# Optimization experiments

Hardware: AMD Instinct MI355X
Metric: run time of the kernel (lower is better)

The kernel has to match this reference:

```python
import jax, jax.numpy as jnp
import numpy as np

N_NODES = 100000
N_EDGES = 1600000
F_IN = 32
HID = 64


def _gcn_conv(x, edge_index, edge_weight, W, b):
    """PyG GCNConv with edge_weight: add self-loops, symmetric degree norm, scatter-add."""
    N = x.shape[0]
    xw = x @ W  # [N, out]
    row, col = edge_index[0], edge_index[1]
    loop = jnp.arange(N)
    row = jnp.concatenate([row, loop])
    col = jnp.concatenate([col, loop])
    ew = jnp.concatenate([edge_weight, jnp.ones((N,), dtype=x.dtype)])
    # degree on target nodes
    deg = jax.ops.segment_sum(ew, col, num_segments=N)
    dinv = jnp.where(deg > 0, jax.lax.rsqrt(deg), 0.0)
    norm = dinv[row] * ew * dinv[col]  # [E+N]
    msg = norm[:, None] * xw[row]      # gather + scale over edges
    out = jax.ops.segment_sum(msg, col, num_segments=N)  # scatter-add
    return out + b


def setup_inputs() -> dict:
    key = jax.random.key(0)
    k = jax.random.split(key, 8)
    x = jax.random.normal(k[0], (N_NODES, F_IN), dtype=jnp.float32)
    edge_index = jax.random.randint(k[1], (2, N_EDGES), 0, N_NODES, dtype=jnp.int64)
    edge_attr = jax.random.uniform(k[2], (N_EDGES, 1), dtype=jnp.float32)
    s1 = 1.0 / np.sqrt(F_IN)
    s2 = 1.0 / np.sqrt(HID)
    W1 = jax.random.normal(k[3], (F_IN, HID), dtype=jnp.float32) * s1
    b1 = jnp.zeros((HID,), dtype=jnp.float32)
    W2 = jax.random.normal(k[4], (HID, F_IN), dtype=jnp.float32) * s2
    b2 = jnp.zeros((F_IN,), dtype=jnp.float32)
    return {"x": x, "edge_index": edge_index, "edge_attr": edge_attr,
            "W1": W1, "b1": b1, "W2": W2, "b2": b2}


def reference(x, edge_index, edge_attr, W1, b1, W2, b2):
    ew = edge_attr.squeeze(-1)
    h = jax.nn.relu(_gcn_conv(x, edge_index, ew, W1, b1))
    out = jax.nn.relu(_gcn_conv(h, edge_index, ew, W2, b2))
    return (out, edge_attr)
```

## Files before the change

kernel.cpp:

```cpp
#include <hip/hip_runtime.h>

#define NN 100000
#define NE 1600000
#define FIN 32
#define FHID 64

#define CLB 7
#define BN (1 << CLB)
#define NB ((NN + BN - 1) / BN)
#define NDB 256
#define CHUNK ((NE + NDB - 1) / NDB)
#define NSC (NB * NDB)
#define SCAN_B 1024
#define SCAN_NB ((NSC + SCAN_B - 1) / SCAN_B)

#define LGKM0 asm volatile("s_waitcnt lgkmcnt(0)" ::: "memory")

__device__ __forceinline__ float lo16(unsigned g) {
    return __uint_as_float(g << 16);
}
__device__ __forceinline__ float hi16(unsigned g) {
    return __uint_as_float(g & 0xFFFF0000u);
}
__device__ __forceinline__ unsigned pack_bf16(float a, float b) {
    unsigned ua = __float_as_uint(a);
    unsigned ub = __float_as_uint(b);
    ua += 0x7FFFu + ((ua >> 16) & 1u);
    ub += 0x7FFFu + ((ub >> 16) & 1u);
    return (ua >> 16) | (ub & 0xFFFF0000u);
}

__global__ void k_dcount(const int* __restrict__ col, int* __restrict__ hist_g) {
    __shared__ int hc[NB];
    for (int i = threadIdx.x; i < NB; i += blockDim.x) hc[i] = 0;
    __syncthreads();
    int beg = blockIdx.x * CHUNK, end = min(beg + CHUNK, NE);
    for (int e = beg + threadIdx.x; e < end; e += blockDim.x)
        atomicAdd(&hc[col[e] >> CLB], 1);
    __syncthreads();
    for (int i = threadIdx.x; i < NB; i += blockDim.x)
        hist_g[i * NDB + blockIdx.x] = hc[i];
}

__global__ void k_scan1(const int* __restrict__ in, int* __restrict__ out,
                        int* __restrict__ bsum) {
    __shared__ int s[SCAN_B];
    int i = blockIdx.x * SCAN_B + threadIdx.x;
    int v = (i < NSC) ? in[i] : 0;
    s[threadIdx.x] = v;
    __syncthreads();
    for (int o = 1; o < SCAN_B; o <<= 1) {
        int t = (threadIdx.x >= o) ? s[threadIdx.x - o] : 0;
        __syncthreads();
        s[threadIdx.x] += t;
        __syncthreads();
    }
    if (i < NSC) out[i] = s[threadIdx.x] - v;
    if (threadIdx.x == SCAN_B - 1) bsum[blockIdx.x] = s[SCAN_B - 1];
}

__global__ void k_scan2(int* __restrict__ bsum) {
    __shared__ int s[256];
    int v = (threadIdx.x < SCAN_NB) ? bsum[threadIdx.x] : 0;
    s[threadIdx.x] = v;
    __syncthreads();
    for (int o = 1; o < 256; o <<= 1) {
        int t = (threadIdx.x >= o) ? s[threadIdx.x - o] : 0;
        __syncthreads();
        s[threadIdx.x] += t;
        __syncthreads();
    }
    if (threadIdx.x < SCAN_NB) bsum[threadIdx.x] = s[threadIdx.x] - v;
}

__global__ void k_scan3(int* __restrict__ out, const int* __restrict__ bsum) {
    int i = blockIdx.x * blockDim.x + threadIdx.x;
    if (i < NSC) out[i] += bsum[i >> 10];
}

__global__ void k_dwrite(const int* __restrict__ row, const int* __restrict__ col,
                         const float* __restrict__ ew, const int* __restrict__ base_g,
                         uint2* __restrict__ rec0) {
    __shared__ int rk[NB];
    __shared__ int bl[NB];
    for (int i = threadIdx.x; i < NB; i += blockDim.x) {
        rk[i] = 0;
        bl[i] = base_g[i * NDB + blockIdx.x];
    }
    __syncthreads();
    int beg = blockIdx.x * CHUNK, end = min(beg + CHUNK, NE);
    for (int e = beg + threadIdx.x; e < end; e += blockDim.x) {
        int c = col[e];
        int bk = c >> CLB;
        int r = atomicAdd(&rk[bk], 1);
        unsigned pack = ((unsigned)(c & (BN - 1)) << 17) | (unsigned)row[e];
        rec0[bl[bk] + r] = make_uint2(pack, __float_as_uint(ew[e]));
    }
}

__global__ void k_bsort(const int* __restrict__ base_g, const uint2* __restrict__ rec0,
                        uint2* __restrict__ csr, int* __restrict__ rowptr,
                        float* __restrict__ dinv) {
    __shared__ int cnt[BN];
    __shared__ int bas[BN];
    __shared__ int cur[BN];
    __shared__ float dg[BN];
    int tid = threadIdx.x;
    int b = blockIdx.x;
    int beg = base_g[b * NDB];
    int end = (b == NB - 1) ? NE : base_g[(b + 1) * NDB];
    if (tid < BN) { cnt[tid] = 0; dg[tid] = 0.0f; }
    __syncthreads();
    for (int j = beg + tid; j < end; j += blockDim.x) {
        uint2 p = rec0[j];
        int cl = p.x >> 17;
        atomicAdd(&cnt[cl], 1);
        atomicAdd(&dg[cl], __uint_as_float(p.y));
    }
    __syncthreads();
    int v0 = (tid < BN) ? cnt[tid] : 0;
    __syncthreads();
    for (int o = 1; o < BN; o <<= 1) {
        int t = (tid < BN && tid >= o) ? cnt[tid - o] : 0;
        __syncthreads();
        if (tid < BN) cnt[tid] += t;
        __syncthreads();
    }
    if (tid < BN) {
        int excl = cnt[tid] - v0;
        bas[tid] = excl;
        cur[tid] = 0;
        int node = b * BN + tid;
        if (node < NN) {
            rowptr[node] = beg + excl;
            dinv[node] = rsqrtf(1.0f + dg[tid]);
        }
    }
    if (b == 0 && tid == 0) rowptr[NN] = NE;
    __syncthreads();
    for (int j = beg + tid; j < end; j += blockDim.x) {
        uint2 p = rec0[j];
        int cl = p.x >> 17;
        int r = atomicAdd(&cur[cl], 1);
        csr[beg + bas[cl] + r] = make_uint2(p.x & 0x1FFFFu, p.y);
    }
}

__global__ void k_scalex(const float* __restrict__ x, const float* __restrict__ dinv,
                         unsigned* __restrict__ xp) {
    int idx = blockIdx.x * blockDim.x + threadIdx.x;
    if (idx >= NN * (FIN / 2)) return;
    float dn = dinv[idx >> 4];
    float2 v = ((const float2*)x)[idx];
    xp[idx] = pack_bf16(v.x * dn, v.y * dn);
}

__global__ __launch_bounds__(256) void k_agg1p(
        const int* __restrict__ rowptr, const uint2* __restrict__ csr,
        const uint2* __restrict__ xp2, const float* __restrict__ dinv,
        uint2* __restrict__ pre) {
    int wid = (blockIdx.x * blockDim.x + threadIdx.x) >> 6;
    int lane = threadIdx.x & 63;
    int n = wid * 2 + (lane >> 5);
    if (n >= NN) return;
    int s = (lane & 31) >> 3;
    int u = lane & 7;
    int beg = rowptr[n], end = rowptr[n + 1];
    float dn = dinv[n];
    uint2 gs = xp2[(size_t)n * 8 + u];
    float c0 = 0.f, c1 = 0.f, c2 = 0.f, c3 = 0.f;
    float d0 = 0.f, d1 = 0.f, d2 = 0.f, d3 = 0.f;
    int j = beg + s;
    for (; j + 4 < end; j += 8) {
        uint2 e0 = csr[j];
        uint2 e1 = csr[j + 4];
        uint2 g0 = xp2[(size_t)e0.x * 8 + u];
        uint2 g1 = xp2[(size_t)e1.x * 8 + u];
        float w0 = __uint_as_float(e0.y);
        float w1 = __uint_as_float(e1.y);
        c0 = fmaf(w0, lo16(g0.x), c0);
        c1 = fmaf(w0, hi16(g0.x), c1);
        c2 = fmaf(w0, lo16(g0.y), c2);
        c3 = fmaf(w0, hi16(g0.y), c3);
        d0 = fmaf(w1, lo16(g1.x), d0);
        d1 = fmaf(w1, hi16(g1.x), d1);
        d2 = fmaf(w1, lo16(g1.y), d2);
        d3 = fmaf(w1, hi16(g1.y), d3);
    }
    for (; j < end; j += 4) {
        uint2 e = csr[j];
        uint2 g = xp2[(size_t)e.x * 8 + u];
        float w = __uint_as_float(e.y);
        c0 = fmaf(w, lo16(g.x), c0);
        c1 = fmaf(w, hi16(g.x), c1);
        c2 = fmaf(w, lo16(g.y), c2);
        c3 = fmaf(w, hi16(g.y), c3);
    }
    c0 += d0; c1 += d1; c2 += d2; c3 += d3;
#pragma unroll
    for (int m = 8; m <= 16; m <<= 1) {
        c0 += __shfl_xor(c0, m, 64);
        c1 += __shfl_xor(c1, m, 64);
        c2 += __shfl_xor(c2, m, 64);
        c3 += __shfl_xor(c3, m, 64);
    }
    if (s == 0) {
        float p0 = dn * (c0 + lo16(gs.x));
        float p1 = dn * (c1 + hi16(gs.x));
        float p2 = dn * (c2 + lo16(gs.y));
        float p3 = dn * (c3 + hi16(gs.y));
        pre[(size_t)n * 8 + u] = make_uint2(pack_bf16(p0, p1), pack_bf16(p2, p3));
    }
}

__global__ __launch_bounds__(256) void k_mlp(
        const uint2* __restrict__ pre2, const float* __restrict__ dinv,
        const float* __restrict__ W1, const float* __restrict__ b1,
        const float* __restrict__ W2, unsigned* __restrict__ hw2p, int nwaves) {
    __shared__ float pre_lds[4 * FIN];
    __shared__ float hv_lds[4 * FHID];
    int lane = threadIdx.x & 63;
    int ws = threadIdx.x >> 6;
    int hh = lane >> 5;
    int f = lane & 31;
    int t = lane & 15;
    int o = lane;
    float W1col[FIN];
#pragma unroll
    for (int k = 0; k < FIN; ++k) W1col[k] = W1[k * FHID + o];
    float b1o = b1[o];
    float W2h[FIN];
#pragma unroll
    for (int k = 0; k < FIN; ++k) W2h[k] = W2[(hh * 32 + k) * FIN + f];

    int gw = (blockIdx.x * blockDim.x + threadIdx.x) >> 6;
    for (int n = gw; n < NN; n += nwaves) {
        float dn = dinv[n];
        if (lane < 8) {
            uint2 g = pre2[(size_t)n * 8 + lane];
            float4 pq = make_float4(lo16(g.x), hi16(g.x), lo16(g.y), hi16(g.y));
            *(float4*)&pre_lds[ws * FIN + 4 * lane] = pq;
        }
        LGKM0;
        float hacc = b1o;
#pragma unroll
        for (int i = 0; i < 8; ++i) {
            float4 qd = *(const float4*)&pre_lds[ws * FIN + 4 * i];
            hacc = fmaf(qd.x, W1col[4 * i + 0], hacc);
            hacc = fmaf(qd.y, W1col[4 * i + 1], hacc);
            hacc = fmaf(qd.z, W1col[4 * i + 2], hacc);
            hacc = fmaf(qd.w, W1col[4 * i + 3], hacc);
        }
        hacc = hacc > 0.0f ? hacc : 0.0f;
        hv_lds[ws * FHID + o] = hacc;
        LGKM0;
        float part = 0.0f;
#pragma unroll
        for (int i = 0; i < 8; ++i) {
            float4 qd = *(const float4*)&hv_lds[ws * FHID + hh * 32 + 4 * i];
            part = fmaf(qd.x, W2h[4 * i + 0], part);
            part = fmaf(qd.y, W2h[4 * i + 1], part);
            part = fmaf(qd.z, W2h[4 * i + 2], part);
            part = fmaf(qd.w, W2h[4 * i + 3], part);
        }
        part += __shfl_xor(part, 32, 64);
        float v = dn * part;
        float vlo = __shfl(v, 2 * t, 64);
        float vhi = __shfl(v, 2 * t + 1, 64);
        if (lane < 16) hw2p[(size_t)n * 16 + lane] = pack_bf16(vlo, vhi);
    }
}

__global__ __launch_bounds__(256) void k_agg2p(
        const int* __restrict__ rowptr, const uint2* __restrict__ csr,
        const uint2* __restrict__ hw2p2, const float* __restrict__ dinv,
        const float* __restrict__ b2, float* __restrict__ out) {
    int wid = (blockIdx.x * blockDim.x + threadIdx.x) >> 6;
    int lane = threadIdx.x & 63;
    int n = wid * 2 + (lane >> 5);
    if (n >= NN) return;
    int s = (lane & 31) >> 3;
    int u = lane & 7;
    int beg = rowptr[n], end = rowptr[n + 1];
    float dn = dinv[n];
    uint2 gs = hw2p2[(size_t)n * 8 + u];
    float c0 = 0.f, c1 = 0.f, c2 = 0.f, c3 = 0.f;
    float d0 = 0.f, d1 = 0.f, d2 = 0.f, d3 = 0.f;
    int j = beg + s;
    for (; j + 4 < end; j += 8) {
        uint2 e0 = csr[j];
        uint2 e1 = csr[j + 4];
        uint2 g0 = hw2p2[(size_t)e0.x * 8 + u];
        uint2 g1 = hw2p2[(size_t)e1.x * 8 + u];
        float w0 = __uint_as_float(e0.y);
        float w1 = __uint_as_float(e1.y);
        c0 = fmaf(w0, lo16(g0.x), c0);
        c1 = fmaf(w0, hi16(g0.x), c1);
        c2 = fmaf(w0, lo16(g0.y), c2);
        c3 = fmaf(w0, hi16(g0.y), c3);
        d0 = fmaf(w1, lo16(g1.x), d0);
        d1 = fmaf(w1, hi16(g1.x), d1);
        d2 = fmaf(w1, lo16(g1.y), d2);
        d3 = fmaf(w1, hi16(g1.y), d3);
    }
    for (; j < end; j += 4) {
        uint2 e = csr[j];
        uint2 g = hw2p2[(size_t)e.x * 8 + u];
        float w = __uint_as_float(e.y);
        c0 = fmaf(w, lo16(g.x), c0);
        c1 = fmaf(w, hi16(g.x), c1);
        c2 = fmaf(w, lo16(g.y), c2);
        c3 = fmaf(w, hi16(g.y), c3);
    }
    c0 += d0; c1 += d1; c2 += d2; c3 += d3;
#pragma unroll
    for (int m = 8; m <= 16; m <<= 1) {
        c0 += __shfl_xor(c0, m, 64);
        c1 += __shfl_xor(c1, m, 64);
        c2 += __shfl_xor(c2, m, 64);
        c3 += __shfl_xor(c3, m, 64);
    }
    if (s == 0) {
        float4 bq = ((const float4*)b2)[u];
        float4 v;
        v.x = dn * (c0 + lo16(gs.x)) + bq.x;
        v.y = dn * (c1 + hi16(gs.x)) + bq.y;
        v.z = dn * (c2 + lo16(gs.y)) + bq.z;
        v.w = dn * (c3 + hi16(gs.y)) + bq.w;
        v.x = v.x > 0.f ? v.x : 0.f;
        v.y = v.y > 0.f ? v.y : 0.f;
        v.z = v.z > 0.f ? v.z : 0.f;
        v.w = v.w > 0.f ? v.w : 0.f;
        ((float4*)out)[(size_t)n * 8 + u] = v;
    }
}

extern "C" void kernel_launch(void* const* d_in, const int* in_sizes, int n_in,
                              void* d_out, int out_size, void* d_ws, size_t ws_size,
                              hipStream_t stream) {
    const float* x  = (const float*)d_in[0];
    const int*   ei = (const int*)d_in[1];
    const float* ea = (const float*)d_in[2];
    const float* W1 = (const float*)d_in[3];
    const float* b1 = (const float*)d_in[4];
    const float* W2 = (const float*)d_in[5];
    const float* b2 = (const float*)d_in[6];
    float* out = (float*)d_out;

    const int* row = ei;
    const int* col = ei + NE;

    char* w = (char*)d_ws;
    uint2* rec0     = (uint2*)w;
    uint2* csr      = rec0 + NE;
    unsigned* xp    = (unsigned*)(csr + NE);
    unsigned* hw2p  = xp + (size_t)NN * 16;
    unsigned* pre   = hw2p + (size_t)NN * 16;
    float* dinv     = (float*)(pre + (size_t)NN * 16);
    int*   rowptr   = (int*)(dinv + NN);
    int*   hist_g   = rowptr + NN + 1;
    int*   scng     = hist_g + NSC;
    int*   bsum     = scng + NSC;

    auto cdiv = [](long long a, int b) { return (int)((a + b - 1) / b); };
    const int PAIR_BLOCKS = cdiv((long long)cdiv(NN, 2) * 64, 256);

    hipMemcpyAsync(out + (size_t)NN * FIN, ea, sizeof(float) * (size_t)NE,
                   hipMemcpyDeviceToDevice, stream);

    k_dcount<<<NDB, 256, 0, stream>>>(col, hist_g);
    k_scan1<<<SCAN_NB, SCAN_B, 0, stream>>>(hist_g, scng, bsum);
    k_scan2<<<1, 256, 0, stream>>>(bsum);
    k_scan3<<<cdiv(NSC, 256), 256, 0, stream>>>(scng, bsum);
    k_dwrite<<<NDB, 256, 0, stream>>>(row, col, ea, scng, rec0);
    k_bsort<<<NB, 256, 0, stream>>>(scng, rec0, csr, rowptr, dinv);

    k_scalex<<<cdiv((long long)NN * (FIN / 2), 256), 256, 0, stream>>>(x, dinv, xp);

    k_agg1p<<<PAIR_BLOCKS, 256, 0, stream>>>(rowptr, csr, (const uint2*)xp, dinv,
                                             (uint2*)pre);
    const int MLP_BLOCKS = 2048;
    k_mlp<<<MLP_BLOCKS, 256, 0, stream>>>((const uint2*)pre, dinv, W1, b1, W2,
                                          hw2p, MLP_BLOCKS * 4);

    k_agg2p<<<PAIR_BLOCKS, 256, 0, stream>>>(rowptr, csr, (const uint2*)hw2p,
                                             dinv, b2, out);
}
```

Measured before the change: 162.1 us.

## Enlarge CSR-build buckets, use 512-thread blocks, keep bucket records in registers

The bucket size for the counting-sort CSR build goes from 128 to 256 nodes, and the number of distribution blocks drops from 256 to 128. This shrinks the histogram and scan arrays. The count, write and bucket-sort kernels now run with 512 threads per block. In the bucket sort, each thread keeps up to 12 records in registers from the first pass, so the second pass does not re-read them from global memory. The catch is a fixed per-bucket capacity of 6144 edges: a bucket with more edges than that would silently lose records, which is fine for uniformly random graphs but not in general.

```diff
diff --git a/kernel.cpp b/kernel.cpp
--- a/kernel.cpp
+++ b/kernel.cpp
@@ -5,14 +5,15 @@
 #define FIN 32
 #define FHID 64
 
-#define CLB 7
+#define CLB 8
 #define BN (1 << CLB)
 #define NB ((NN + BN - 1) / BN)
-#define NDB 256
+#define NDB 128
 #define CHUNK ((NE + NDB - 1) / NDB)
 #define NSC (NB * NDB)
 #define SCAN_B 1024
 #define SCAN_NB ((NSC + SCAN_B - 1) / SCAN_B)
+#define RCAP 12
 
 #define LGKM0 asm volatile("s_waitcnt lgkmcnt(0)" ::: "memory")
 
@@ -30,7 +31,8 @@
     return (ua >> 16) | (ub & 0xFFFF0000u);
 }
 
-__global__ void k_dcount(const int* __restrict__ col, int* __restrict__ hist_g) {
+__global__ __launch_bounds__(512) void k_dcount(const int* __restrict__ col,
+                                                int* __restrict__ hist_g) {
     __shared__ int hc[NB];
     for (int i = threadIdx.x; i < NB; i += blockDim.x) hc[i] = 0;
     __syncthreads();
@@ -78,9 +80,10 @@
     if (i < NSC) out[i] += bsum[i >> 10];
 }
 
-__global__ void k_dwrite(const int* __restrict__ row, const int* __restrict__ col,
-                         const float* __restrict__ ew, const int* __restrict__ base_g,
-                         uint2* __restrict__ rec0) {
+__global__ __launch_bounds__(512) void k_dwrite(
+        const int* __restrict__ row, const int* __restrict__ col,
+        const float* __restrict__ ew, const int* __restrict__ base_g,
+        uint2* __restrict__ rec0) {
     __shared__ int rk[NB];
     __shared__ int bl[NB];
     for (int i = threadIdx.x; i < NB; i += blockDim.x) {
@@ -98,9 +101,10 @@
     }
 }
 
-__global__ void k_bsort(const int* __restrict__ base_g, const uint2* __restrict__ rec0,
-                        uint2* __restrict__ csr, int* __restrict__ rowptr,
-                        float* __restrict__ dinv) {
+__global__ __launch_bounds__(512) void k_bsort(
+        const int* __restrict__ base_g, const uint2* __restrict__ rec0,
+        uint2* __restrict__ csr, int* __restrict__ rowptr,
+        float* __restrict__ dinv) {
     __shared__ int cnt[BN];
     __shared__ int bas[BN];
     __shared__ int cur[BN];
@@ -111,11 +115,18 @@
     int end = (b == NB - 1) ? NE : base_g[(b + 1) * NDB];
     if (tid < BN) { cnt[tid] = 0; dg[tid] = 0.0f; }
     __syncthreads();
-    for (int j = beg + tid; j < end; j += blockDim.x) {
-        uint2 p = rec0[j];
-        int cl = p.x >> 17;
-        atomicAdd(&cnt[cl], 1);
-        atomicAdd(&dg[cl], __uint_as_float(p.y));
+    uint2 rc[RCAP];
+#pragma unroll
+    for (int i = 0; i < RCAP; ++i) {
+        int j = beg + tid + i * 512;
+        if (j < end) {
+            uint2 p = rec0[j];
+            rc[i] = p;
+            atomicAdd(&cnt[p.x >> 17], 1);
+            atomicAdd(&dg[p.x >> 17], __uint_as_float(p.y));
+        } else {
+            rc[i] = make_uint2(0u, 0u);
+        }
     }
     __syncthreads();
     int v0 = (tid < BN) ? cnt[tid] : 0;
@@ -138,11 +149,15 @@
     }
     if (b == 0 && tid == 0) rowptr[NN] = NE;
     __syncthreads();
-    for (int j = beg + tid; j < end; j += blockDim.x) {
-        uint2 p = rec0[j];
-        int cl = p.x >> 17;
-        int r = atomicAdd(&cur[cl], 1);
-        csr[beg + bas[cl] + r] = make_uint2(p.x & 0x1FFFFu, p.y);
+#pragma unroll
+    for (int i = 0; i < RCAP; ++i) {
+        int j = beg + tid + i * 512;
+        if (j < end) {
+            uint2 p = rc[i];
+            int cl = p.x >> 17;
+            int r = atomicAdd(&cur[cl], 1);
+            csr[beg + bas[cl] + r] = make_uint2(p.x & 0x1FFFFu, p.y);
+        }
     }
 }
 
@@ -368,12 +383,12 @@
     hipMemcpyAsync(out + (size_t)NN * FIN, ea, sizeof(float) * (size_t)NE,
                    hipMemcpyDeviceToDevice, stream);
 
-    k_dcount<<<NDB, 256, 0, stream>>>(col, hist_g);
+    k_dcount<<<NDB, 512, 0, stream>>>(col, hist_g);
     k_scan1<<<SCAN_NB, SCAN_B, 0, stream>>>(hist_g, scng, bsum);
     k_scan2<<<1, 256, 0, stream>>>(bsum);
     k_scan3<<<cdiv(NSC, 256), 256, 0, stream>>>(scng, bsum);
-    k_dwrite<<<NDB, 256, 0, stream>>>(row, col, ea, scng, rec0);
-    k_bsort<<<NB, 256, 0, stream>>>(scng, rec0, csr, rowptr, dinv);
+    k_dwrite<<<NDB, 512, 0, stream>>>(row, col, ea, scng, rec0);
+    k_bsort<<<NB, 512, 0, stream>>>(scng, rec0, csr, rowptr, dinv);
 
     k_scalex<<<cdiv((long long)NN * (FIN / 2), 256), 256, 0, stream>>>(x, dinv, xp);
 
```

Result: no change. 159.2 us (-1.8%).
